# Kernel optimization log

Hardware: AMD Instinct MI355X
Metric: run time of the kernel (lower is better)

Reference implementation:

```python
import jax, jax.numpy as jnp
import numpy as np

DIM = 512
HEADS = 4
DH = 128          # dim_head
CHUNK = 16        # chunk_size
MAX_LR = 0.01     # default_adaptive_step_transform max_lr
EPS = 1e-6        # flax RMSNorm epsilon


def setup_inputs() -> dict:
    key = jax.random.key(0)
    ks = jax.random.split(key, 8)
    B, S = 2, 2048
    dim_inner = HEADS * DH
    seq = jax.random.normal(ks[0], (B, S, DIM), jnp.float32)
    store_norm_scale = jnp.ones((DIM,), jnp.float32)               # RMSNorm scale
    W_kv = (jax.random.normal(ks[1], (DIM, 2 * dim_inner)) * 0.02).astype(jnp.float32)
    W_step = (jax.random.normal(ks[2], (DIM, HEADS)) * 0.02).astype(jnp.float32)
    W_mom = (jax.random.normal(ks[3], (DIM, HEADS)) * 0.02).astype(jnp.float32)
    W_decay = (jax.random.normal(ks[4], (DIM, HEADS)) * 0.02).astype(jnp.float32)
    # past memory-MLP weights, shared init expanded to (b, h, dh, dh)
    w0 = jnp.broadcast_to((jax.random.normal(ks[5], (DH, DH)) * 0.02).astype(jnp.float32), (B, HEADS, DH, DH)) + 0.0
    w1 = jnp.broadcast_to((jax.random.normal(ks[6], (DH, DH)) * 0.02).astype(jnp.float32), (B, HEADS, DH, DH)) + 0.0
    return {"seq": seq, "store_norm_scale": store_norm_scale, "W_kv": W_kv,
            "W_step": W_step, "W_mom": W_mom, "W_decay": W_decay, "w0": w0, "w1": w1}


def _mlp(w0, w1, x):
    # MemoryMLP depth=2: x @ w0 ; silu ; @ w1
    return jax.nn.silu(x @ w0) @ w1


def _chunk_loss(w0, w1, k, lr, v):
    pred = _mlp(w0, w1, k)                       # [c, d]
    return jnp.sum(jnp.mean((pred - v) ** 2, axis=-1) * lr)


def _binop(e1, e2):
    a1, b1 = e1
    a2, b2 = e2
    return a1 * a2, a2 * b1 + b2


def _lin_scan(a, b):
    # first-order linear recurrence y_t = a_t * y_{t-1} + b_t along chunk axis (axis=2)
    return jax.lax.associative_scan(_binop, (a, b), axis=2)[1]


def _store(seq, store_norm_scale, W_kv, W_step, W_mom, W_decay, w0, w1):
    B, S, _ = seq.shape
    n = S // CHUNK
    # pre RMSNorm (with scale)
    x = seq * jax.lax.rsqrt(jnp.mean(seq * seq, axis=-1, keepdims=True) + EPS) * store_norm_scale
    # adaptive per-token lr:  sigmoid(x @ W_step) * max_lr  -> [b, h, s]
    lr = jax.nn.sigmoid(jnp.einsum('bsd,dh->bhs', x, W_step)) * MAX_LR
    # per-chunk mean -> momentum / decay factors  [b, h, n, 1]
    mean = x.reshape(B, n, CHUNK, DIM).mean(axis=2)
    mom = jax.nn.sigmoid(jnp.einsum('bnd,dh->bhn', mean, W_mom))[..., None]
    dec = jax.nn.sigmoid(jnp.einsum('bnd,dh->bhn', mean, W_decay))[..., None]
    # keys / values  [b*h, n, c, dh]
    kv = x @ W_kv
    k, v = jnp.split(kv, 2, axis=-1)
    k = k.reshape(B, n, CHUNK, HEADS, DH).transpose(0, 3, 1, 2, 4).reshape(B * HEADS, n, CHUNK, DH)
    v = v.reshape(B, n, CHUNK, HEADS, DH).transpose(0, 3, 1, 2, 4).reshape(B * HEADS, n, CHUNK, DH)
    lr_ch = lr.reshape(B, HEADS, n, CHUNK).reshape(B * HEADS, n, CHUNK)
    w0bh = w0.reshape(B * HEADS, DH, DH)
    w1bh = w1.reshape(B * HEADS, DH, DH)
    # per-chunk gradients of the MLP loss at the *past* weights (all chunks independent)
    gfn = jax.grad(_chunk_loss, argnums=(0, 1))
    gfn = jax.vmap(gfn, in_axes=(None, None, 0, 0, 0))   # over chunks n
    gfn = jax.vmap(gfn, in_axes=(0, 0, 0, 0, 0))         # over b*h
    g0, g1 = gfn(w0bh, w1bh, k, lr_ch, v)                # [b*h, n, dh, dh]
    s0 = (-g0).reshape(B, HEADS, n, DH * DH)             # surprises
    s1 = (-g1).reshape(B, HEADS, n, DH * DH)
    # momentum scan then decay scan (Titans update rule)
    m0 = _lin_scan(jnp.broadcast_to(mom, s0.shape), s0)
    m1 = _lin_scan(jnp.broadcast_to(mom, s1.shape), s1)
    u0 = _lin_scan(jnp.broadcast_to(1.0 - dec, m0.shape), m0)
    u1 = _lin_scan(jnp.broadcast_to(1.0 - dec, m1.shape), m1)
    updates = jnp.stack([u0.reshape(B, HEADS, n, DH, DH),
                         u1.reshape(B, HEADS, n, DH, DH)], axis=0)  # [2, b, h, n, dh, dh]
    return updates


def reference(seq, store_norm_scale, W_kv, W_step, W_mom, W_decay, w0, w1):
    return _store(seq, store_norm_scale, W_kv, W_step, W_mom, W_decay, w0, w1)
```

## Files before the change

### kernel.cpp

```cpp
#include <hip/hip_runtime.h>

#define DIMX 512
#define HEADSX 4
#define DHX 128
#define CHX 16
#define NCX 128
#define SX 2048
#define BX 2
#define BHX 8
#define PADX 520
#define PADF 136

typedef unsigned short ushort_t;
typedef unsigned int uint_t;
typedef short bf16x8 __attribute__((ext_vector_type(8)));
typedef float f32x4 __attribute__((ext_vector_type(4)));

__device__ __forceinline__ float sigmoidf_(float z){ return 1.0f/(1.0f + __expf(-z)); }

__device__ __forceinline__ ushort_t f2bf(float f){
  uint_t u = __float_as_uint(f);
  return (ushort_t)((u + 0x7FFFu + ((u >> 16) & 1u)) >> 16);
}
__device__ __forceinline__ uint_t pk2(float a, float b){
  return (uint_t)f2bf(a) | ((uint_t)f2bf(b) << 16);
}

__global__ __launch_bounds__(256) void k_prep(const float* __restrict__ Wkv,
    const float* __restrict__ w0, const float* __restrict__ w1,
    const float* __restrict__ scale,
    const float* __restrict__ Wstep, const float* __restrict__ Wmom,
    const float* __restrict__ Wdec,
    ushort_t* __restrict__ WkvT, ushort_t* __restrict__ w0T,
    ushort_t* __restrict__ w1T, ushort_t* __restrict__ w1n,
    float* __restrict__ wfsS, float* __restrict__ wfsM, float* __restrict__ wfsD){
  int blk = blockIdx.x; int tid = threadIdx.x;
  if (blk < 64){
    int h = blk >> 4, kt = blk & 15;
    __shared__ ushort_t tile[256][33];
    for (int i=tid; i<8192; i+=256){
      int kk = i >> 8, col = i & 255;
      int wcol = (col < 128) ? (h*128 + col) : (384 + h*128 + col);
      float v = Wkv[(size_t)(kt*32+kk)*1024 + wcol];
      tile[col][kk] = f2bf(v);
    }
    __syncthreads();
    for (int i=tid; i<8192; i+=256){
      int col = i >> 5, kk = i & 31;
      WkvT[(((size_t)h*16 + kt)*256 + col)*32 + kk] = tile[col][kk];
    }
  } else if (blk < 72){
    int bh = blk - 64;
    size_t base = (size_t)bh*16384;
    for (int i=tid; i<16384; i+=256){
      int r = i >> 7, c = i & 127;
      w0T[base + i] = f2bf(w0[base + (size_t)c*128 + r]);
      w1T[base + i] = f2bf(w1[base + (size_t)c*128 + r]);
      w1n[base + i] = f2bf(w1[base + i]);
    }
  } else {
    for (int i=tid; i<2048; i+=256){
      int d = i & 511, h = i >> 9;
      float sc = scale[d];
      wfsS[i] = sc * Wstep[d*4 + h];
      wfsM[i] = sc * Wmom [d*4 + h];
      wfsD[i] = sc * Wdec [d*4 + h];
    }
  }
}

__global__ __launch_bounds__(1024, 4) void k_fused5(const float* __restrict__ seq,
    const float* __restrict__ scale,
    const float* __restrict__ wfsS, const float* __restrict__ wfsM,
    const float* __restrict__ wfsD,
    const ushort_t* __restrict__ WkvT, const ushort_t* __restrict__ w0T,
    const ushort_t* __restrict__ w1T, const ushort_t* __restrict__ w1n,
    ushort_t* __restrict__ fac0, ushort_t* __restrict__ fac1,
    float* __restrict__ momw, float* __restrict__ decw){
  int blk = blockIdx.x;
  int bh = blk & 7, t4 = blk >> 3;
  int b = bh >> 2, h = bh & 3;
  int tid = threadIdx.x;
  int wv = tid >> 6;
  int mi = wv >> 2, ni = wv & 3;
  int lane = tid & 63;
  int quad = lane >> 4, nl = lane & 15;
  int tid_g = ni*64 + lane;
  int t = t4*4 + mi;
  int bt = bh*NCX + t;
  const f32x4 zero = {0.f,0.f,0.f,0.f};

  __shared__ __align__(16) ushort_t xs[4][16*PADX];
  __shared__ __align__(16) ushort_t ks[4][16*PADF];
  __shared__ __align__(16) ushort_t as_[4][16*PADF];
  __shared__ __align__(16) ushort_t dp_[4][16*PADF];
  __shared__ float lr_s[4][16];
  __shared__ float red_m[4][4], red_d[4][4];

  {
    int c = tid_g >> 4, sl = tid_g & 15;
    const float4* sr = (const float4*)(seq + ((size_t)(b*SX + t*CHX) + c)*DIMX);
    const float4* scl = (const float4*)scale;
    const float4* wS = (const float4*)(wfsS + h*512);
    const float4* wM = (const float4*)(wfsM + h*512);
    const float4* wD = (const float4*)(wfsD + h*512);
    float4 q[8];
    #pragma unroll
    for (int jj=0; jj<8; jj++) q[jj] = sr[sl + 16*jj];
    float ss=0.f, lp=0.f, pm=0.f, pd=0.f;
    #pragma unroll
    for (int jj=0; jj<8; jj++){
      float4 a = q[jj];
      float4 s4 = wS[sl+16*jj], m4 = wM[sl+16*jj], d4 = wD[sl+16*jj];
      ss += a.x*a.x + a.y*a.y + a.z*a.z + a.w*a.w;
      lp += a.x*s4.x + a.y*s4.y + a.z*s4.z + a.w*s4.w;
      pm += a.x*m4.x + a.y*m4.y + a.z*m4.z + a.w*m4.w;
      pd += a.x*d4.x + a.y*d4.y + a.z*d4.z + a.w*d4.w;
    }
    #pragma unroll
    for (int mk=1; mk<16; mk<<=1){
      ss += __shfl_xor(ss,mk,64); lp += __shfl_xor(lp,mk,64);
      pm += __shfl_xor(pm,mk,64); pd += __shfl_xor(pd,mk,64);
    }
    float rs = 1.0f / sqrtf(ss*(1.0f/DIMX) + 1e-6f);
    if (sl==0) lr_s[mi][c] = 0.01f * sigmoidf_(rs*lp);
    float pmr = rs*pm, pdr = rs*pd;
    #pragma unroll
    for (int mk=16; mk<64; mk<<=1){ pmr += __shfl_xor(pmr,mk,64); pdr += __shfl_xor(pdr,mk,64); }
    if (lane==0){ red_m[mi][ni]=pmr; red_d[mi][ni]=pdr; }
    #pragma unroll
    for (int jj=0; jj<8; jj++){
      float4 s4 = scl[sl+16*jj];
      uint2 u;
      u.x = pk2(q[jj].x*rs*s4.x, q[jj].y*rs*s4.y);
      u.y = pk2(q[jj].z*rs*s4.z, q[jj].w*rs*s4.w);
      *(uint2*)&xs[mi][c*PADX + (sl+16*jj)*4] = u;
    }
  }
  __syncthreads();
  if (tid_g==0){
    momw[bt] = sigmoidf_((red_m[mi][0]+red_m[mi][1]+red_m[mi][2]+red_m[mi][3])*(1.0f/CHX));
    decw[bt] = 1.0f - sigmoidf_((red_d[mi][0]+red_d[mi][1]+red_d[mi][2]+red_d[mi][3])*(1.0f/CHX));
  }

  f32x4 kacc[2] = {zero,zero};
  f32x4 vacc[2] = {zero,zero};
  const ushort_t* wkvh = WkvT + (size_t)h*16*256*32;
  for (int kt=0; kt<16; kt++){
    bf16x8 Af = *(const bf16x8*)&xs[mi][nl*PADX + kt*32 + quad*8];
    #pragma unroll
    for (int s=0; s<2; s++){
      int ktile = 2*ni + s;
      bf16x8 Bk = *(const bf16x8*)&wkvh[((size_t)kt*256 + (ktile*16+nl))*32 + quad*8];
      kacc[s] = __builtin_amdgcn_mfma_f32_16x16x32_bf16(Af, Bk, kacc[s], 0,0,0);
      int vtile = 8 + 2*ni + s;
      bf16x8 Bv = *(const bf16x8*)&wkvh[((size_t)kt*256 + (vtile*16+nl))*32 + quad*8];
      vacc[s] = __builtin_amdgcn_mfma_f32_16x16x32_bf16(Af, Bv, vacc[s], 0,0,0);
    }
  }
  #pragma unroll
  for (int s=0;s<2;s++){
    #pragma unroll
    for (int r=0;r<4;r++)
      ks[mi][(quad*4+r)*PADF + 32*ni + 16*s + nl] = f2bf(kacc[s][r]);
  }
  __syncthreads();

  const ushort_t* w0b = w0T + (size_t)bh*16384;
  f32x4 hacc[2] = {zero,zero};
  #pragma unroll
  for (int kt=0; kt<4; kt++){
    bf16x8 Af = *(const bf16x8*)&ks[mi][nl*PADF + kt*32 + quad*8];
    #pragma unroll
    for (int s=0; s<2; s++){
      int n0 = (2*ni+s)*16;
      bf16x8 Bf = *(const bf16x8*)&w0b[(size_t)(n0+nl)*128 + kt*32 + quad*8];
      hacc[s] = __builtin_amdgcn_mfma_f32_16x16x32_bf16(Af, Bf, hacc[s], 0,0,0);
    }
  }
  float sp[2][4];
  #pragma unroll
  for (int s=0;s<2;s++){
    #pragma unroll
    for (int r=0;r<4;r++){
      float hh = hacc[s][r];
      float sg = sigmoidf_(hh);
      sp[s][r] = sg*(1.0f + hh*(1.0f-sg));
      as_[mi][(quad*4+r)*PADF + 32*ni + 16*s + nl] = f2bf(hh*sg);
    }
  }
  __syncthreads();

  const ushort_t* w1tb = w1T + (size_t)bh*16384;
  f32x4 pacc[2] = {zero,zero};
  #pragma unroll
  for (int kt=0; kt<4; kt++){
    bf16x8 Af = *(const bf16x8*)&as_[mi][nl*PADF + kt*32 + quad*8];
    #pragma unroll
    for (int s=0; s<2; s++){
      int n0 = (2*ni+s)*16;
      bf16x8 Bf = *(const bf16x8*)&w1tb[(size_t)(n0+nl)*128 + kt*32 + quad*8];
      pacc[s] = __builtin_amdgcn_mfma_f32_16x16x32_bf16(Af, Bf, pacc[s], 0,0,0);
    }
  }
  float lrv[4];
  #pragma unroll
  for (int r=0;r<4;r++) lrv[r] = lr_s[mi][quad*4 + r];
  #pragma unroll
  for (int s=0;s<2;s++){
    #pragma unroll
    for (int r=0;r<4;r++){
      float dp = (2.0f/DHX)*lrv[r]*(pacc[s][r] - vacc[s][r]);
      dp_[mi][(quad*4+r)*PADF + 32*ni + 16*s + nl] = f2bf(dp);
    }
  }
  if (tid_g < 128){
    int p = tid_g;
    ushort_t rowv[32];
    #pragma unroll
    for (int c=0;c<16;c++){ rowv[c] = ks[mi][c*PADF + p]; rowv[16+c] = as_[mi][c*PADF + p]; }
    uint4* dq = (uint4*)(fac0 + ((size_t)bt*128 + p)*32);
    const uint4* rv = (const uint4*)rowv;
    dq[0]=rv[0]; dq[1]=rv[1]; dq[2]=rv[2]; dq[3]=rv[3];
  }
  __syncthreads();

  const ushort_t* w1nb = w1n + (size_t)bh*16384;
  f32x4 dacc[2] = {zero,zero};
  #pragma unroll
  for (int kt=0; kt<4; kt++){
    bf16x8 Af = *(const bf16x8*)&dp_[mi][nl*PADF + kt*32 + quad*8];
    #pragma unroll
    for (int s=0; s<2; s++){
      int n0 = (2*ni+s)*16;
      bf16x8 Bf = *(const bf16x8*)&w1nb[(size_t)(n0+nl)*128 + kt*32 + quad*8];
      dacc[s] = __builtin_amdgcn_mfma_f32_16x16x32_bf16(Af, Bf, dacc[s], 0,0,0);
    }
  }
  #pragma unroll
  for (int s=0;s<2;s++){
    #pragma unroll
    for (int r=0;r<4;r++)
      ks[mi][(quad*4+r)*PADF + 32*ni + 16*s + nl] = f2bf(dacc[s][r]*sp[s][r]);
  }
  __syncthreads();

  if (tid_g < 128){
    int p = tid_g;
    ushort_t rowv[32];
    #pragma unroll
    for (int c=0;c<16;c++){ rowv[c] = ks[mi][c*PADF + p]; rowv[16+c] = dp_[mi][c*PADF + p]; }
    uint4* dq = (uint4*)(fac1 + ((size_t)bt*128 + p)*32);
    const uint4* rv = (const uint4*)rowv;
    dq[0]=rv[0]; dq[1]=rv[1]; dq[2]=rv[2]; dq[3]=rv[3];
  }
}

__global__ __launch_bounds__(64) void k_scan3(const ushort_t* __restrict__ fac0,
    const ushort_t* __restrict__ fac1,
    const float* __restrict__ momw, const float* __restrict__ decw,
    float* __restrict__ out){
  int blk = blockIdx.x;
  int bh  = blk & 7;
  int jb  = (blk >> 3) & 7;
  int ig  = (blk >> 6) & 7;
  int mat = blk >> 9;
  int lane = threadIdx.x;
  int quad = lane >> 4, rrow = lane & 15;
  const f32x4 zero = {0.f,0.f,0.f,0.f};
  const bf16x8 fz = {0,0,0,0,0,0,0,0};

  size_t rowbase = (size_t)bh*NCX*128;
  const ushort_t* pa = fac0 + (rowbase + (size_t)(ig*16 + rrow))*32 + mat*16 + quad*8;
  const ushort_t* pb = fac1 + (rowbase + (size_t)(jb*16 + rrow))*32 + mat*16 + quad*8;
  bool act = (quad < 2);

  bf16x8 fa0=fz, fb0=fz, fa1=fz, fb1=fz;
  if (act){
    fa0 = *(const bf16x8*)(pa);
    fb0 = *(const bf16x8*)(pb);
    fa1 = *(const bf16x8*)(pa + 4096);
    fb1 = *(const bf16x8*)(pb + 4096);
  }

  f32x4 m_ = zero, u_ = zero;
  size_t obase = ((size_t)(mat*BHX + bh)*NCX)*((size_t)DHX*DHX)
               + (size_t)(ig*16 + quad*4)*DHX + (size_t)(jb*16 + rrow);
  const float* mop = momw + bh*NCX;
  const float* dep = decw + bh*NCX;

  for (int t=0; t<NCX; t+=2){
    bf16x8 na0=fz, nb0=fz, na1=fz, nb1=fz;
    if (act && (t+2 < NCX)){
      na0 = *(const bf16x8*)(pa + (size_t)(t+2)*4096);
      nb0 = *(const bf16x8*)(pb + (size_t)(t+2)*4096);
      na1 = *(const bf16x8*)(pa + (size_t)(t+3)*4096);
      nb1 = *(const bf16x8*)(pb + (size_t)(t+3)*4096);
    }
    float mo = mop[t], de = dep[t];
    f32x4 g = __builtin_amdgcn_mfma_f32_16x16x32_bf16(fa0, fb0, zero, 0,0,0);
    float* ob = out + obase + (size_t)t*(DHX*DHX);
    #pragma unroll
    for (int r=0;r<4;r++){
      m_[r] = mo*m_[r] - g[r];
      u_[r] = de*u_[r] + m_[r];
      ob[(size_t)r*DHX] = u_[r];
    }
    mo = mop[t+1]; de = dep[t+1];
    g = __builtin_amdgcn_mfma_f32_16x16x32_bf16(fa1, fb1, zero, 0,0,0);
    ob += (size_t)DHX*DHX;
    #pragma unroll
    for (int r=0;r<4;r++){
      m_[r] = mo*m_[r] - g[r];
      u_[r] = de*u_[r] + m_[r];
      ob[(size_t)r*DHX] = u_[r];
    }
    fa0=na0; fb0=nb0; fa1=na1; fb1=nb1;
  }
}

extern "C" void kernel_launch(void* const* d_in, const int* in_sizes, int n_in,
                              void* d_out, int out_size, void* d_ws, size_t ws_size,
                              hipStream_t stream) {
  (void)in_sizes; (void)n_in; (void)out_size; (void)ws_size;
  const float* seq   = (const float*)d_in[0];
  const float* scale = (const float*)d_in[1];
  const float* Wkv   = (const float*)d_in[2];
  const float* Wstep = (const float*)d_in[3];
  const float* Wmom  = (const float*)d_in[4];
  const float* Wdec  = (const float*)d_in[5];
  const float* w0    = (const float*)d_in[6];
  const float* w1    = (const float*)d_in[7];
  float* out = (float*)d_out;
  float* ws  = (float*)d_ws;

  ushort_t* fac0 = (ushort_t*)(ws);
  ushort_t* fac1 = (ushort_t*)(ws + 2097152);
  ushort_t* WkvT = (ushort_t*)(ws + 4194304);
  ushort_t* w0T  = (ushort_t*)(ws + 4456448);
  ushort_t* w1T  = (ushort_t*)(ws + 4521984);
  ushort_t* w1n  = (ushort_t*)(ws + 4587520);
  float*    momw = ws + 4653056;
  float*    decw = ws + 4654080;
  float*    wfsS = ws + 4655104;
  float*    wfsM = ws + 4657152;
  float*    wfsD = ws + 4659200;

  k_prep<<<dim3(73), dim3(256), 0, stream>>>(Wkv, w0, w1, scale, Wstep, Wmom, Wdec,
      WkvT, w0T, w1T, w1n, wfsS, wfsM, wfsD);
  k_fused5<<<dim3(256), dim3(1024), 0, stream>>>(seq, scale, wfsS, wfsM, wfsD,
      WkvT, w0T, w1T, w1n, fac0, fac1, momw, decw);
  k_scan3<<<dim3(1024), dim3(64), 0, stream>>>(fac0, fac1, momw, decw, out);
}
```

Before: 236.0 us.

## Fuse gradient and scan kernels into one pipelined kernel with atomic batch flags

Merges the per-chunk gradient kernel and the momentum/decay scan kernel into a single launch. Producer blocks process chunks in four time batches and signal completion through per-(bh,batch) atomic counters. Consumer blocks spin-wait on each counter and then scan that batch, so scan output writes overlap with gradient compute. This relies on producer and consumer blocks being co-resident to avoid deadlock, and it reorganises the producer work into 256-thread blocks that each loop over 4 chunks.

```diff
diff --git a/kernel.cpp b/kernel.cpp
--- a/kernel.cpp
+++ b/kernel.cpp
@@ -10,6 +10,8 @@
 #define BHX 8
 #define PADX 520
 #define PADF 136
+#define NBAT 4
+#define BATCH 32
 
 typedef unsigned short ushort_t;
 typedef unsigned int uint_t;
@@ -33,7 +35,8 @@
     const float* __restrict__ Wdec,
     ushort_t* __restrict__ WkvT, ushort_t* __restrict__ w0T,
     ushort_t* __restrict__ w1T, ushort_t* __restrict__ w1n,
-    float* __restrict__ wfsS, float* __restrict__ wfsM, float* __restrict__ wfsD){
+    float* __restrict__ wfsS, float* __restrict__ wfsM, float* __restrict__ wfsD,
+    uint_t* done){
   int blk = blockIdx.x; int tid = threadIdx.x;
   if (blk < 64){
     int h = blk >> 4, kt = blk & 15;
@@ -66,256 +69,268 @@
       wfsM[i] = sc * Wmom [d*4 + h];
       wfsD[i] = sc * Wdec [d*4 + h];
     }
+    if (tid < BHX*NBAT)
+      __hip_atomic_store(&done[tid], 0u, __ATOMIC_RELAXED, __HIP_MEMORY_SCOPE_AGENT);
   }
 }
 
-__global__ __launch_bounds__(1024, 4) void k_fused5(const float* __restrict__ seq,
+__global__ __launch_bounds__(256, 2) void k_pipe(const float* __restrict__ seq,
     const float* __restrict__ scale,
     const float* __restrict__ wfsS, const float* __restrict__ wfsM,
     const float* __restrict__ wfsD,
     const ushort_t* __restrict__ WkvT, const ushort_t* __restrict__ w0T,
     const ushort_t* __restrict__ w1T, const ushort_t* __restrict__ w1n,
     ushort_t* __restrict__ fac0, ushort_t* __restrict__ fac1,
-    float* __restrict__ momw, float* __restrict__ decw){
+    float* __restrict__ momw, float* __restrict__ decw,
+    uint_t* done, float* __restrict__ out){
+  __shared__ __align__(16) ushort_t xs[16*PADX];
+  __shared__ __align__(16) ushort_t ks[16*PADF];
+  __shared__ __align__(16) ushort_t as_[16*PADF];
+  __shared__ __align__(16) ushort_t dp_[16*PADF];
+  __shared__ __align__(16) ushort_t dh_[16*PADF];
+  __shared__ float lr_s[16];
+  __shared__ float red_m[4], red_d[4];
   int blk = blockIdx.x;
-  int bh = blk & 7, t4 = blk >> 3;
-  int b = bh >> 2, h = bh & 3;
   int tid = threadIdx.x;
-  int wv = tid >> 6;
-  int mi = wv >> 2, ni = wv & 3;
-  int lane = tid & 63;
-  int quad = lane >> 4, nl = lane & 15;
-  int tid_g = ni*64 + lane;
-  int t = t4*4 + mi;
-  int bt = bh*NCX + t;
   const f32x4 zero = {0.f,0.f,0.f,0.f};
 
-  __shared__ __align__(16) ushort_t xs[4][16*PADX];
-  __shared__ __align__(16) ushort_t ks[4][16*PADF];
-  __shared__ __align__(16) ushort_t as_[4][16*PADF];
-  __shared__ __align__(16) ushort_t dp_[4][16*PADF];
-  __shared__ float lr_s[4][16];
-  __shared__ float red_m[4][4], red_d[4][4];
-
-  {
-    int c = tid_g >> 4, sl = tid_g & 15;
-    const float4* sr = (const float4*)(seq + ((size_t)(b*SX + t*CHX) + c)*DIMX);
-    const float4* scl = (const float4*)scale;
-    const float4* wS = (const float4*)(wfsS + h*512);
-    const float4* wM = (const float4*)(wfsM + h*512);
-    const float4* wD = (const float4*)(wfsD + h*512);
-    float4 q[8];
-    #pragma unroll
-    for (int jj=0; jj<8; jj++) q[jj] = sr[sl + 16*jj];
-    float ss=0.f, lp=0.f, pm=0.f, pd=0.f;
-    #pragma unroll
-    for (int jj=0; jj<8; jj++){
-      float4 a = q[jj];
-      float4 s4 = wS[sl+16*jj], m4 = wM[sl+16*jj], d4 = wD[sl+16*jj];
-      ss += a.x*a.x + a.y*a.y + a.z*a.z + a.w*a.w;
-      lp += a.x*s4.x + a.y*s4.y + a.z*s4.z + a.w*s4.w;
-      pm += a.x*m4.x + a.y*m4.y + a.z*m4.z + a.w*m4.w;
-      pd += a.x*d4.x + a.y*d4.y + a.z*d4.z + a.w*d4.w;
-    }
-    #pragma unroll
-    for (int mk=1; mk<16; mk<<=1){
-      ss += __shfl_xor(ss,mk,64); lp += __shfl_xor(lp,mk,64);
-      pm += __shfl_xor(pm,mk,64); pd += __shfl_xor(pd,mk,64);
-    }
-    float rs = 1.0f / sqrtf(ss*(1.0f/DIMX) + 1e-6f);
-    if (sl==0) lr_s[mi][c] = 0.01f * sigmoidf_(rs*lp);
-    float pmr = rs*pm, pdr = rs*pd;
-    #pragma unroll
-    for (int mk=16; mk<64; mk<<=1){ pmr += __shfl_xor(pmr,mk,64); pdr += __shfl_xor(pdr,mk,64); }
-    if (lane==0){ red_m[mi][ni]=pmr; red_d[mi][ni]=pdr; }
-    #pragma unroll
-    for (int jj=0; jj<8; jj++){
-      float4 s4 = scl[sl+16*jj];
-      uint2 u;
-      u.x = pk2(q[jj].x*rs*s4.x, q[jj].y*rs*s4.y);
-      u.y = pk2(q[jj].z*rs*s4.z, q[jj].w*rs*s4.w);
-      *(uint2*)&xs[mi][c*PADX + (sl+16*jj)*4] = u;
-    }
-  }
-  __syncthreads();
-  if (tid_g==0){
-    momw[bt] = sigmoidf_((red_m[mi][0]+red_m[mi][1]+red_m[mi][2]+red_m[mi][3])*(1.0f/CHX));
-    decw[bt] = 1.0f - sigmoidf_((red_d[mi][0]+red_d[mi][1]+red_d[mi][2]+red_d[mi][3])*(1.0f/CHX));
-  }
-
-  f32x4 kacc[2] = {zero,zero};
-  f32x4 vacc[2] = {zero,zero};
-  const ushort_t* wkvh = WkvT + (size_t)h*16*256*32;
-  for (int kt=0; kt<16; kt++){
-    bf16x8 Af = *(const bf16x8*)&xs[mi][nl*PADX + kt*32 + quad*8];
-    #pragma unroll
-    for (int s=0; s<2; s++){
-      int ktile = 2*ni + s;
-      bf16x8 Bk = *(const bf16x8*)&wkvh[((size_t)kt*256 + (ktile*16+nl))*32 + quad*8];
-      kacc[s] = __builtin_amdgcn_mfma_f32_16x16x32_bf16(Af, Bk, kacc[s], 0,0,0);
-      int vtile = 8 + 2*ni + s;
-      bf16x8 Bv = *(const bf16x8*)&wkvh[((size_t)kt*256 + (vtile*16+nl))*32 + quad*8];
-      vacc[s] = __builtin_amdgcn_mfma_f32_16x16x32_bf16(Af, Bv, vacc[s], 0,0,0);
-    }
-  }
-  #pragma unroll
-  for (int s=0;s<2;s++){
-    #pragma unroll
-    for (int r=0;r<4;r++)
-      ks[mi][(quad*4+r)*PADF + 32*ni + 16*s + nl] = f2bf(kacc[s][r]);
-  }
-  __syncthreads();
-
-  const ushort_t* w0b = w0T + (size_t)bh*16384;
-  f32x4 hacc[2] = {zero,zero};
-  #pragma unroll
-  for (int kt=0; kt<4; kt++){
-    bf16x8 Af = *(const bf16x8*)&ks[mi][nl*PADF + kt*32 + quad*8];
-    #pragma unroll
-    for (int s=0; s<2; s++){
-      int n0 = (2*ni+s)*16;
-      bf16x8 Bf = *(const bf16x8*)&w0b[(size_t)(n0+nl)*128 + kt*32 + quad*8];
-      hacc[s] = __builtin_amdgcn_mfma_f32_16x16x32_bf16(Af, Bf, hacc[s], 0,0,0);
-    }
-  }
-  float sp[2][4];
-  #pragma unroll
-  for (int s=0;s<2;s++){
-    #pragma unroll
-    for (int r=0;r<4;r++){
-      float hh = hacc[s][r];
-      float sg = sigmoidf_(hh);
-      sp[s][r] = sg*(1.0f + hh*(1.0f-sg));
-      as_[mi][(quad*4+r)*PADF + 32*ni + 16*s + nl] = f2bf(hh*sg);
-    }
-  }
-  __syncthreads();
-
-  const ushort_t* w1tb = w1T + (size_t)bh*16384;
-  f32x4 pacc[2] = {zero,zero};
-  #pragma unroll
-  for (int kt=0; kt<4; kt++){
-    bf16x8 Af = *(const bf16x8*)&as_[mi][nl*PADF + kt*32 + quad*8];
-    #pragma unroll
-    for (int s=0; s<2; s++){
-      int n0 = (2*ni+s)*16;
-      bf16x8 Bf = *(const bf16x8*)&w1tb[(size_t)(n0+nl)*128 + kt*32 + quad*8];
-      pacc[s] = __builtin_amdgcn_mfma_f32_16x16x32_bf16(Af, Bf, pacc[s], 0,0,0);
-    }
-  }
-  float lrv[4];
-  #pragma unroll
-  for (int r=0;r<4;r++) lrv[r] = lr_s[mi][quad*4 + r];
-  #pragma unroll
-  for (int s=0;s<2;s++){
-    #pragma unroll
-    for (int r=0;r<4;r++){
-      float dp = (2.0f/DHX)*lrv[r]*(pacc[s][r] - vacc[s][r]);
-      dp_[mi][(quad*4+r)*PADF + 32*ni + 16*s + nl] = f2bf(dp);
-    }
-  }
-  if (tid_g < 128){
-    int p = tid_g;
-    ushort_t rowv[32];
-    #pragma unroll
-    for (int c=0;c<16;c++){ rowv[c] = ks[mi][c*PADF + p]; rowv[16+c] = as_[mi][c*PADF + p]; }
-    uint4* dq = (uint4*)(fac0 + ((size_t)bt*128 + p)*32);
-    const uint4* rv = (const uint4*)rowv;
-    dq[0]=rv[0]; dq[1]=rv[1]; dq[2]=rv[2]; dq[3]=rv[3];
-  }
-  __syncthreads();
-
-  const ushort_t* w1nb = w1n + (size_t)bh*16384;
-  f32x4 dacc[2] = {zero,zero};
-  #pragma unroll
-  for (int kt=0; kt<4; kt++){
-    bf16x8 Af = *(const bf16x8*)&dp_[mi][nl*PADF + kt*32 + quad*8];
-    #pragma unroll
-    for (int s=0; s<2; s++){
-      int n0 = (2*ni+s)*16;
-      bf16x8 Bf = *(const bf16x8*)&w1nb[(size_t)(n0+nl)*128 + kt*32 + quad*8];
-      dacc[s] = __builtin_amdgcn_mfma_f32_16x16x32_bf16(Af, Bf, dacc[s], 0,0,0);
-    }
-  }
-  #pragma unroll
-  for (int s=0;s<2;s++){
-    #pragma unroll
-    for (int r=0;r<4;r++)
-      ks[mi][(quad*4+r)*PADF + 32*ni + 16*s + nl] = f2bf(dacc[s][r]*sp[s][r]);
-  }
-  __syncthreads();
-
-  if (tid_g < 128){
-    int p = tid_g;
-    ushort_t rowv[32];
-    #pragma unroll
-    for (int c=0;c<16;c++){ rowv[c] = ks[mi][c*PADF + p]; rowv[16+c] = dp_[mi][c*PADF + p]; }
-    uint4* dq = (uint4*)(fac1 + ((size_t)bt*128 + p)*32);
-    const uint4* rv = (const uint4*)rowv;
-    dq[0]=rv[0]; dq[1]=rv[1]; dq[2]=rv[2]; dq[3]=rv[3];
-  }
-}
-
-__global__ __launch_bounds__(64) void k_scan3(const ushort_t* __restrict__ fac0,
-    const ushort_t* __restrict__ fac1,
-    const float* __restrict__ momw, const float* __restrict__ decw,
-    float* __restrict__ out){
-  int blk = blockIdx.x;
-  int bh  = blk & 7;
-  int jb  = (blk >> 3) & 7;
-  int ig  = (blk >> 6) & 7;
-  int mat = blk >> 9;
-  int lane = threadIdx.x;
-  int quad = lane >> 4, rrow = lane & 15;
-  const f32x4 zero = {0.f,0.f,0.f,0.f};
-  const bf16x8 fz = {0,0,0,0,0,0,0,0};
-
-  size_t rowbase = (size_t)bh*NCX*128;
-  const ushort_t* pa = fac0 + (rowbase + (size_t)(ig*16 + rrow))*32 + mat*16 + quad*8;
-  const ushort_t* pb = fac1 + (rowbase + (size_t)(jb*16 + rrow))*32 + mat*16 + quad*8;
-  bool act = (quad < 2);
-
-  bf16x8 fa0=fz, fb0=fz, fa1=fz, fb1=fz;
-  if (act){
-    fa0 = *(const bf16x8*)(pa);
-    fb0 = *(const bf16x8*)(pb);
-    fa1 = *(const bf16x8*)(pa + 4096);
-    fb1 = *(const bf16x8*)(pb + 4096);
-  }
-
-  f32x4 m_ = zero, u_ = zero;
-  size_t obase = ((size_t)(mat*BHX + bh)*NCX)*((size_t)DHX*DHX)
-               + (size_t)(ig*16 + quad*4)*DHX + (size_t)(jb*16 + rrow);
-  const float* mop = momw + bh*NCX;
-  const float* dep = decw + bh*NCX;
-
-  for (int t=0; t<NCX; t+=2){
-    bf16x8 na0=fz, nb0=fz, na1=fz, nb1=fz;
-    if (act && (t+2 < NCX)){
-      na0 = *(const bf16x8*)(pa + (size_t)(t+2)*4096);
-      nb0 = *(const bf16x8*)(pb + (size_t)(t+2)*4096);
-      na1 = *(const bf16x8*)(pa + (size_t)(t+3)*4096);
-      nb1 = *(const bf16x8*)(pb + (size_t)(t+3)*4096);
-    }
-    float mo = mop[t], de = dep[t];
-    f32x4 g = __builtin_amdgcn_mfma_f32_16x16x32_bf16(fa0, fb0, zero, 0,0,0);
-    float* ob = out + obase + (size_t)t*(DHX*DHX);
-    #pragma unroll
-    for (int r=0;r<4;r++){
-      m_[r] = mo*m_[r] - g[r];
-      u_[r] = de*u_[r] + m_[r];
-      ob[(size_t)r*DHX] = u_[r];
-    }
-    mo = mop[t+1]; de = dep[t+1];
-    g = __builtin_amdgcn_mfma_f32_16x16x32_bf16(fa1, fb1, zero, 0,0,0);
-    ob += (size_t)DHX*DHX;
-    #pragma unroll
-    for (int r=0;r<4;r++){
-      m_[r] = mo*m_[r] - g[r];
-      u_[r] = de*u_[r] + m_[r];
-      ob[(size_t)r*DHX] = u_[r];
-    }
-    fa0=na0; fb0=nb0; fa1=na1; fb1=nb1;
+  if (blk < 256){
+    int bh = blk & 7, g = blk >> 3;
+    int b = bh >> 2, h = bh & 3;
+    int wv = tid >> 6, lane = tid & 63;
+    int quad = lane >> 4, nl = lane & 15;
+
+    for (int it=0; it<4; it++){
+      int t = g + 32*it;
+      int bt = bh*NCX + t;
+
+      {
+        int c = tid >> 4, sl = tid & 15;
+        const float4* sr = (const float4*)(seq + ((size_t)(b*SX + t*CHX) + c)*DIMX);
+        const float4* scl = (const float4*)scale;
+        const float4* wS = (const float4*)(wfsS + h*512);
+        const float4* wM = (const float4*)(wfsM + h*512);
+        const float4* wD = (const float4*)(wfsD + h*512);
+        float4 q[8];
+        #pragma unroll
+        for (int jj=0; jj<8; jj++) q[jj] = sr[sl + 16*jj];
+        float ss=0.f, lp=0.f, pm=0.f, pd=0.f;
+        #pragma unroll
+        for (int jj=0; jj<8; jj++){
+          float4 a = q[jj];
+          float4 s4 = wS[sl+16*jj], m4 = wM[sl+16*jj], d4 = wD[sl+16*jj];
+          ss += a.x*a.x + a.y*a.y + a.z*a.z + a.w*a.w;
+          lp += a.x*s4.x + a.y*s4.y + a.z*s4.z + a.w*s4.w;
+          pm += a.x*m4.x + a.y*m4.y + a.z*m4.z + a.w*m4.w;
+          pd += a.x*d4.x + a.y*d4.y + a.z*d4.z + a.w*d4.w;
+        }
+        #pragma unroll
+        for (int mk=1; mk<16; mk<<=1){
+          ss += __shfl_xor(ss,mk,64); lp += __shfl_xor(lp,mk,64);
+          pm += __shfl_xor(pm,mk,64); pd += __shfl_xor(pd,mk,64);
+        }
+        float rs = 1.0f / sqrtf(ss*(1.0f/DIMX) + 1e-6f);
+        if (sl==0) lr_s[c] = 0.01f * sigmoidf_(rs*lp);
+        float pmr = rs*pm, pdr = rs*pd;
+        #pragma unroll
+        for (int mk=16; mk<64; mk<<=1){ pmr += __shfl_xor(pmr,mk,64); pdr += __shfl_xor(pdr,mk,64); }
+        if (lane==0){ red_m[wv]=pmr; red_d[wv]=pdr; }
+        #pragma unroll
+        for (int jj=0; jj<8; jj++){
+          float4 s4 = scl[sl+16*jj];
+          uint2 u;
+          u.x = pk2(q[jj].x*rs*s4.x, q[jj].y*rs*s4.y);
+          u.y = pk2(q[jj].z*rs*s4.z, q[jj].w*rs*s4.w);
+          *(uint2*)&xs[c*PADX + (sl+16*jj)*4] = u;
+        }
+      }
+      __syncthreads();
+      if (tid==0){
+        momw[bt] = sigmoidf_((red_m[0]+red_m[1]+red_m[2]+red_m[3])*(1.0f/CHX));
+        decw[bt] = 1.0f - sigmoidf_((red_d[0]+red_d[1]+red_d[2]+red_d[3])*(1.0f/CHX));
+      }
+
+      f32x4 kacc[2] = {zero,zero};
+      f32x4 vacc[2] = {zero,zero};
+      const ushort_t* wkvh = WkvT + (size_t)h*16*256*32;
+      for (int kt=0; kt<16; kt++){
+        bf16x8 Af = *(const bf16x8*)&xs[nl*PADX + kt*32 + quad*8];
+        #pragma unroll
+        for (int s=0; s<2; s++){
+          int ktile = 2*wv + s;
+          bf16x8 Bk = *(const bf16x8*)&wkvh[((size_t)kt*256 + (ktile*16+nl))*32 + quad*8];
+          kacc[s] = __builtin_amdgcn_mfma_f32_16x16x32_bf16(Af, Bk, kacc[s], 0,0,0);
+          int vtile = 8 + 2*wv + s;
+          bf16x8 Bv = *(const bf16x8*)&wkvh[((size_t)kt*256 + (vtile*16+nl))*32 + quad*8];
+          vacc[s] = __builtin_amdgcn_mfma_f32_16x16x32_bf16(Af, Bv, vacc[s], 0,0,0);
+        }
+      }
+      #pragma unroll
+      for (int s=0;s<2;s++){
+        #pragma unroll
+        for (int r=0;r<4;r++)
+          ks[(quad*4+r)*PADF + 32*wv + 16*s + nl] = f2bf(kacc[s][r]);
+      }
+      __syncthreads();
+
+      const ushort_t* w0b = w0T + (size_t)bh*16384;
+      f32x4 hacc[2] = {zero,zero};
+      #pragma unroll
+      for (int kt=0; kt<4; kt++){
+        bf16x8 Af = *(const bf16x8*)&ks[nl*PADF + kt*32 + quad*8];
+        #pragma unroll
+        for (int s=0; s<2; s++){
+          int n0 = (2*wv+s)*16;
+          bf16x8 Bf = *(const bf16x8*)&w0b[(size_t)(n0+nl)*128 + kt*32 + quad*8];
+          hacc[s] = __builtin_amdgcn_mfma_f32_16x16x32_bf16(Af, Bf, hacc[s], 0,0,0);
+        }
+      }
+      float sp[2][4];
+      #pragma unroll
+      for (int s=0;s<2;s++){
+        #pragma unroll
+        for (int r=0;r<4;r++){
+          float hh = hacc[s][r];
+          float sg = sigmoidf_(hh);
+          sp[s][r] = sg*(1.0f + hh*(1.0f-sg));
+          as_[(quad*4+r)*PADF + 32*wv + 16*s + nl] = f2bf(hh*sg);
+        }
+      }
+      __syncthreads();
+
+      const ushort_t* w1tb = w1T + (size_t)bh*16384;
+      f32x4 pacc[2] = {zero,zero};
+      #pragma unroll
+      for (int kt=0; kt<4; kt++){
+        bf16x8 Af = *(const bf16x8*)&as_[nl*PADF + kt*32 + quad*8];
+        #pragma unroll
+        for (int s=0; s<2; s++){
+          int n0 = (2*wv+s)*16;
+          bf16x8 Bf = *(const bf16x8*)&w1tb[(size_t)(n0+nl)*128 + kt*32 + quad*8];
+          pacc[s] = __builtin_amdgcn_mfma_f32_16x16x32_bf16(Af, Bf, pacc[s], 0,0,0);
+        }
+      }
+      float lrv[4];
+      #pragma unroll
+      for (int r=0;r<4;r++) lrv[r] = lr_s[quad*4 + r];
+      #pragma unroll
+      for (int s=0;s<2;s++){
+        #pragma unroll
+        for (int r=0;r<4;r++){
+          float dp = (2.0f/DHX)*lrv[r]*(pacc[s][r] - vacc[s][r]);
+          dp_[(quad*4+r)*PADF + 32*wv + 16*s + nl] = f2bf(dp);
+        }
+      }
+      if (tid < 128){
+        int p = tid;
+        ushort_t rowv[32];
+        #pragma unroll
+        for (int c=0;c<16;c++){ rowv[c] = ks[c*PADF + p]; rowv[16+c] = as_[c*PADF + p]; }
+        uint4* dq = (uint4*)(fac0 + ((size_t)bt*128 + p)*32);
+        const uint4* rv = (const uint4*)rowv;
+        dq[0]=rv[0]; dq[1]=rv[1]; dq[2]=rv[2]; dq[3]=rv[3];
+      }
+      __syncthreads();
+
+      const ushort_t* w1nb = w1n + (size_t)bh*16384;
+      f32x4 dacc[2] = {zero,zero};
+      #pragma unroll
+      for (int kt=0; kt<4; kt++){
+        bf16x8 Af = *(const bf16x8*)&dp_[nl*PADF + kt*32 + quad*8];
+        #pragma unroll
+        for (int s=0; s<2; s++){
+          int n0 = (2*wv+s)*16;
+          bf16x8 Bf = *(const bf16x8*)&w1nb[(size_t)(n0+nl)*128 + kt*32 + quad*8];
+          dacc[s] = __builtin_amdgcn_mfma_f32_16x16x32_bf16(Af, Bf, dacc[s], 0,0,0);
+        }
+      }
+      #pragma unroll
+      for (int s=0;s<2;s++){
+        #pragma unroll
+        for (int r=0;r<4;r++)
+          dh_[(quad*4+r)*PADF + 32*wv + 16*s + nl] = f2bf(dacc[s][r]*sp[s][r]);
+      }
+      __syncthreads();
+
+      if (tid < 128){
+        int p = tid;
+        ushort_t rowv[32];
+        #pragma unroll
+        for (int c=0;c<16;c++){ rowv[c] = dh_[c*PADF + p]; rowv[16+c] = dp_[c*PADF + p]; }
+        uint4* dq = (uint4*)(fac1 + ((size_t)bt*128 + p)*32);
+        const uint4* rv = (const uint4*)rowv;
+        dq[0]=rv[0]; dq[1]=rv[1]; dq[2]=rv[2]; dq[3]=rv[3];
+      }
+      __syncthreads();
+      if (tid==0)
+        __hip_atomic_fetch_add(&done[bh*NBAT + it], 1u,
+                               __ATOMIC_RELEASE, __HIP_MEMORY_SCOPE_AGENT);
+    }
+  } else {
+    int cblk = blk - 256;
+    int wv = tid >> 6, lane = tid & 63;
+    int task = cblk*4 + wv;
+    int bh  = task & 7;
+    int jb  = (task >> 3) & 7;
+    int ig  = (task >> 6) & 7;
+    int mat = task >> 9;
+    int quad = lane >> 4, rrow = lane & 15;
+    const bf16x8 fz = {0,0,0,0,0,0,0,0};
+
+    size_t rowbase = (size_t)bh*NCX*128;
+    const ushort_t* pa = fac0 + (rowbase + (size_t)(ig*16 + rrow))*32 + mat*16 + quad*8;
+    const ushort_t* pb = fac1 + (rowbase + (size_t)(jb*16 + rrow))*32 + mat*16 + quad*8;
+    bool act = (quad < 2);
+
+    f32x4 m_ = zero, u_ = zero;
+    size_t obase = ((size_t)(mat*BHX + bh)*NCX)*((size_t)DHX*DHX)
+                 + (size_t)(ig*16 + quad*4)*DHX + (size_t)(jb*16 + rrow);
+    const float* mop = momw + bh*NCX;
+    const float* dep = decw + bh*NCX;
+
+    for (int bat=0; bat<NBAT; bat++){
+      int t0 = bat*BATCH;
+      while (__hip_atomic_load(&done[bh*NBAT + bat], __ATOMIC_RELAXED,
+                               __HIP_MEMORY_SCOPE_AGENT) < 32u)
+        __builtin_amdgcn_s_sleep(8);
+      __builtin_amdgcn_fence(__ATOMIC_ACQUIRE, "agent");
+
+      bf16x8 fa0=fz, fb0=fz, fa1=fz, fb1=fz;
+      if (act){
+        fa0 = *(const bf16x8*)(pa + (size_t)t0*4096);
+        fb0 = *(const bf16x8*)(pb + (size_t)t0*4096);
+        fa1 = *(const bf16x8*)(pa + (size_t)(t0+1)*4096);
+        fb1 = *(const bf16x8*)(pb + (size_t)(t0+1)*4096);
+      }
+      for (int t=t0; t<t0+BATCH; t+=2){
+        bf16x8 na0=fz, nb0=fz, na1=fz, nb1=fz;
+        if (act && (t+2 < t0+BATCH)){
+          na0 = *(const bf16x8*)(pa + (size_t)(t+2)*4096);
+          nb0 = *(const bf16x8*)(pb + (size_t)(t+2)*4096);
+          na1 = *(const bf16x8*)(pa + (size_t)(t+3)*4096);
+          nb1 = *(const bf16x8*)(pb + (size_t)(t+3)*4096);
+        }
+        float mo = mop[t], de = dep[t];
+        f32x4 gg = __builtin_amdgcn_mfma_f32_16x16x32_bf16(fa0, fb0, zero, 0,0,0);
+        float* ob = out + obase + (size_t)t*(DHX*DHX);
+        #pragma unroll
+        for (int r=0;r<4;r++){
+          m_[r] = mo*m_[r] - gg[r];
+          u_[r] = de*u_[r] + m_[r];
+          ob[(size_t)r*DHX] = u_[r];
+        }
+        mo = mop[t+1]; de = dep[t+1];
+        gg = __builtin_amdgcn_mfma_f32_16x16x32_bf16(fa1, fb1, zero, 0,0,0);
+        ob += (size_t)DHX*DHX;
+        #pragma unroll
+        for (int r=0;r<4;r++){
+          m_[r] = mo*m_[r] - gg[r];
+          u_[r] = de*u_[r] + m_[r];
+          ob[(size_t)r*DHX] = u_[r];
+        }
+        fa0=na0; fb0=nb0; fa1=na1; fb1=nb1;
+      }
+    }
   }
 }
 
@@ -345,10 +360,10 @@
   float*    wfsS = ws + 4655104;
   float*    wfsM = ws + 4657152;
   float*    wfsD = ws + 4659200;
+  uint_t*   done = (uint_t*)(ws + 4661248);
 
   k_prep<<<dim3(73), dim3(256), 0, stream>>>(Wkv, w0, w1, scale, Wstep, Wmom, Wdec,
-      WkvT, w0T, w1T, w1n, wfsS, wfsM, wfsD);
-  k_fused5<<<dim3(256), dim3(1024), 0, stream>>>(seq, scale, wfsS, wfsM, wfsD,
-      WkvT, w0T, w1T, w1n, fac0, fac1, momw, decw);
-  k_scan3<<<dim3(1024), dim3(64), 0, stream>>>(fac0, fac1, momw, decw, out);
-}
+      WkvT, w0T, w1T, w1n, wfsS, wfsM, wfsD, done);
+  k_pipe<<<dim3(512), dim3(256), 0, stream>>>(seq, scale, wfsS, wfsM, wfsD,
+      WkvT, w0T, w1T, w1n, fac0, fac1, momw, decw, done, out);
+}
```

Result: slower. 457.4 us (+93.8%).
